# Optimization experiments

Hardware: AMD Instinct MI355X
Metric: run time of the kernel (lower is better)

The kernel has to match this reference:

```python
import jax, jax.numpy as jnp
import numpy as np

EMB = 256
N_NODES = 20000
N_EDGES = 200000


def _sage_layer(x, src, dst, edge_attr, W, b, n_nodes):
    # message = x[src] + edge_attr ; mean-aggregate into dst ; ReLU(Linear([x;agg]))
    msg = x[src] + edge_attr                                   # [2E, emb]
    s = jax.ops.segment_sum(msg, dst, num_segments=n_nodes)    # [N, emb]
    cnt = jax.ops.segment_sum(jnp.ones((dst.shape[0], 1), x.dtype), dst,
                              num_segments=n_nodes)            # [N, 1]
    agg = s / jnp.maximum(cnt, 1.0)
    return jax.nn.relu(jnp.concatenate([x, agg], axis=1) @ W + b)


def setup_inputs() -> dict:
    key = jax.random.key(0)
    ks = jax.random.split(key, 12)
    sc = 0.05
    inp = {
        "x": jax.random.normal(ks[0], (N_NODES, EMB), jnp.float32),
        "edge_attr": jax.random.normal(ks[1], (N_EDGES, EMB), jnp.float32),
        "batch_q_embds": jax.random.normal(ks[2], (N_EDGES, EMB), jnp.float32),
        "edge_index": jax.random.randint(ks[3], (2, N_EDGES), 0, N_NODES, jnp.int64
                                         if jax.config.jax_enable_x64 else jnp.int32),
        "W_rev1": jax.random.normal(ks[4], (EMB, EMB), jnp.float32) * sc,
        "b_rev1": jnp.zeros((EMB,), jnp.float32),
        "W_rev2": jax.random.normal(ks[5], (EMB, EMB), jnp.float32) * sc,
        "b_rev2": jnp.zeros((EMB,), jnp.float32),
        "W_sage1": jax.random.normal(ks[6], (2 * EMB, EMB), jnp.float32) * sc,
        "b_sage1": jnp.zeros((EMB,), jnp.float32),
        "W_sage2": jax.random.normal(ks[7], (2 * EMB, EMB), jnp.float32) * sc,
        "b_sage2": jnp.zeros((EMB,), jnp.float32),
        "W_pred1": jax.random.normal(ks[8], (6 * EMB, EMB), jnp.float32) * sc,
        "b_pred1": jnp.zeros((EMB,), jnp.float32),
        "W_pred2": jax.random.normal(ks[9], (EMB, 1), jnp.float32) * sc,
        "b_pred2": jnp.zeros((1,), jnp.float32),
    }
    return inp


def reference(x, edge_attr, batch_q_embds, edge_index,
              W_rev1, b_rev1, W_rev2, b_rev2,
              W_sage1, b_sage1, W_sage2, b_sage2,
              W_pred1, b_pred1, W_pred2, b_pred2):
    src, dst = edge_index[0], edge_index[1]
    # reverse-edge attributes via proj_reverse MLP
    edge_attr_rev = jax.nn.relu(edge_attr @ W_rev1 + b_rev1) @ W_rev2 + b_rev2
    src_f = jnp.concatenate([src, dst])          # [2E]
    dst_f = jnp.concatenate([dst, src])          # [2E]
    ea_f = jnp.concatenate([edge_attr, edge_attr_rev], axis=0)  # [2E, emb]
    # 2-layer GraphSAGE backbone over nodes, collect per-layer outputs
    h1 = _sage_layer(x, src_f, dst_f, ea_f, W_sage1, b_sage1, N_NODES)
    h2 = _sage_layer(h1, src_f, dst_f, ea_f, W_sage2, b_sage2, N_NODES)
    h_e = jnp.concatenate([h1, h2], axis=1)      # [N, 2*emb]
    # per-edge triple features: [q ; h_e[head] ; edge_attr ; h_e[tail]]
    h_triple = jnp.concatenate([batch_q_embds, h_e[src], edge_attr, h_e[dst]], axis=1)
    attn_logits = (jax.nn.relu(h_triple @ W_pred1 + b_pred1) @ W_pred2 + b_pred2)[:, 0]
    # idp-bern sampling (training=True): gumbel-like logistic noise, temp=1
    u = jax.random.uniform(jax.random.key(42), attn_logits.shape,
                           attn_logits.dtype, 1e-10, 1.0 - 1e-10)
    noise = jnp.log(u) - jnp.log(1.0 - u)
    sampled = jax.nn.sigmoid(attn_logits + noise)
    return attn_logits, sampled
```

## Files before the change

kernel.cpp:

```cpp
#include <hip/hip_runtime.h>
#include <cstdint>
#include <cstddef>

#define EMB 256
#define NN 20000
#define NE 200000
#define NE2 400000

typedef unsigned short ushort_t;
typedef __attribute__((ext_vector_type(8))) short bf16x8;
typedef __attribute__((ext_vector_type(4))) float f32x4;

__device__ __forceinline__ ushort_t f2bf(float f) {
    unsigned u = __float_as_uint(f);
    u += 0x7FFFu + ((u >> 16) & 1u);
    return (ushort_t)(u >> 16);
}
__device__ __forceinline__ float bf2f(ushort_t u) {
    return __uint_as_float(((unsigned)u) << 16);
}

__device__ __forceinline__ void async_cp16(const ushort_t* g, ushort_t* l) {
    __builtin_amdgcn_global_load_lds(
        (const __attribute__((address_space(1))) unsigned int*)g,
        (__attribute__((address_space(3))) unsigned int*)l,
        16, 0, 0);
}

__device__ __forceinline__ void pc_map(int bid, int T, int& p, int& colblk) {
    int Tf = T & ~15;
    if (bid < Tf) {
        p = (bid >> 4) * 8 + (bid & 7);
        colblk = (bid >> 3) & 1;
    } else {
        int rem = bid - Tf;
        int nr = (T - Tf) >> 1;
        p = (T >> 1) - nr + rem % nr;
        colblk = rem / nr;
    }
}

__device__ __forceinline__ unsigned rotl32(unsigned v, int d) {
    return (v << d) | (v >> (32 - d));
}
__device__ __forceinline__ void threefry2x32(unsigned k0, unsigned k1,
                                             unsigned x0, unsigned x1,
                                             unsigned& o0, unsigned& o1) {
    unsigned k2 = k0 ^ k1 ^ 0x1BD11BDAu;
    x0 += k0; x1 += k1;
#define TF_R(r) { x0 += x1; x1 = rotl32(x1, (r)); x1 ^= x0; }
    TF_R(13) TF_R(15) TF_R(26) TF_R(6)
    x0 += k1; x1 += k2 + 1u;
    TF_R(17) TF_R(29) TF_R(16) TF_R(24)
    x0 += k2; x1 += k0 + 2u;
    TF_R(13) TF_R(15) TF_R(26) TF_R(6)
    x0 += k0; x1 += k1 + 3u;
    TF_R(17) TF_R(29) TF_R(16) TF_R(24)
    x0 += k1; x1 += k2 + 4u;
    TF_R(13) TF_R(15) TF_R(26) TF_R(6)
    x0 += k2; x1 += k0 + 5u;
#undef TF_R
    o0 = x0; o1 = x1;
}

__global__ void deg_kernel(const int* __restrict__ src, const int* __restrict__ dst,
                           int* __restrict__ deg) {
    int i = blockIdx.x * blockDim.x + threadIdx.x;
    if (i < NE2) {
        int n = (i < NE) ? dst[i] : src[i - NE];
        atomicAdd(&deg[n], 1);
    }
}

__global__ void prefix_kernel(const int* __restrict__ deg, int* __restrict__ row_start,
                              int* __restrict__ cursor) {
    __shared__ int sums[1024];
    int t = threadIdx.x;
    const int CH = (NN + 1023) / 1024;
    int lo = t * CH, hi = lo + CH;
    if (hi > NN) hi = NN;
    if (lo > NN) lo = NN;
    int s = 0;
    for (int n = lo; n < hi; n++) s += deg[n];
    sums[t] = s;
    __syncthreads();
    for (int off = 1; off < 1024; off <<= 1) {
        int v = (t >= off) ? sums[t - off] : 0;
        __syncthreads();
        sums[t] += v;
        __syncthreads();
    }
    int run = (t == 0) ? 0 : sums[t - 1];
    for (int n = lo; n < hi; n++) {
        row_start[n] = run;
        cursor[n] = run;
        run += deg[n];
    }
    if (t == 1023) row_start[NN] = sums[1023];
}

__global__ void scatter_kernel(const int* __restrict__ src, const int* __restrict__ dst,
                               int* __restrict__ cursor, int* __restrict__ elist) {
    int i = blockIdx.x * blockDim.x + threadIdx.x;
    if (i < NE2) {
        int n = (i < NE) ? dst[i] : src[i - NE];
        int pos = atomicAdd(&cursor[n], 1);
        elist[pos] = i;
    }
}

__global__ void conv2_kernel(const float* __restrict__ a, ushort_t* __restrict__ oa, int na8,
                             const float* __restrict__ b, ushort_t* __restrict__ ob, int nb8) {
    int i = blockIdx.x * 256 + threadIdx.x;
    const float* p;
    ushort_t* o;
    if (i < na8) { p = a + (size_t)i * 8; o = oa + (size_t)i * 8; }
    else {
        int j = i - na8;
        if (j >= nb8) return;
        p = b + (size_t)j * 8; o = ob + (size_t)j * 8;
    }
    float4 u = *(const float4*)p;
    float4 v = *(const float4*)(p + 4);
    union { ushort_t s[8]; uint4 w; } r;
    r.s[0] = f2bf(u.x); r.s[1] = f2bf(u.y); r.s[2] = f2bf(u.z); r.s[3] = f2bf(u.w);
    r.s[4] = f2bf(v.x); r.s[5] = f2bf(v.y); r.s[6] = f2bf(v.z); r.s[7] = f2bf(v.w);
    *(uint4*)o = r.w;
}

struct TD { const float* src; ushort_t* dst; int stride, koff, kr; };
struct TA { TD d[8]; };

__global__ void transpose_all_kernel(TA ta) {
    TD t = ta.d[blockIdx.y];
    int k = blockIdx.x;
    if (k >= t.kr) return;
    int n = threadIdx.x;
    t.dst[(size_t)n * t.stride + t.koff + k] = f2bf(t.src[(size_t)k * 256 + n]);
}

template <int KTOT, int EPI, bool A0F32>
__global__ __launch_bounds__(256, 4) void mfma_gemm(
        const void* __restrict__ A0v, int rsA0,
        const ushort_t* __restrict__ A1, int rsA1,
        const ushort_t* __restrict__ Bt, const ushort_t* __restrict__ Bt2,
        const float* __restrict__ bias,
        void* __restrict__ out, void* __restrict__ out2, int rsOut, int M,
        const int* __restrict__ srcp, const int* __restrict__ dstp,
        const float* __restrict__ Hs, const float* __restrict__ Hd,
        const float* __restrict__ w2) {
    __shared__ ushort_t As[2][128 * 32];
    __shared__ ushort_t Bs[2][128 * 32];
    __shared__ float red[128];

    int tid = threadIdx.x;
    int lane = tid & 63;
    int wave = tid >> 6;
    int wr = wave >> 1;
    int wc = wave & 1;
    int quad = lane >> 4;
    int col_l = lane & 15;
    int p, colblk;
    pc_map(blockIdx.x, gridDim.x, p, colblk);

    const ushort_t* Bsel = blockIdx.y ? Bt2 : Bt;
    void* Osel = blockIdx.y ? out2 : out;

    f32x4 acc[4][4];
#pragma unroll
    for (int mt = 0; mt < 4; mt++)
#pragma unroll
        for (int nt = 0; nt < 4; nt++) acc[mt][nt] = (f32x4)0.f;

    for (int k0 = 0; k0 < KTOT; k0 += 64) {
        __syncthreads();
#pragma unroll
        for (int h = 0; h < 2; h++) {
            int kk = k0 + 32 * h;
#pragma unroll
            for (int j = 0; j < 2; j++) {
                int flat = tid + 256 * j;
                int n = flat >> 2, ch = flat & 3;
                const ushort_t* gp = Bsel + (size_t)(colblk * 128 + n) * KTOT + kk + ch * 8;
                async_cp16(gp, Bs[h] + ((wave * 64 + 256 * j) * 8));
            }
            bool seg1 = (KTOT == 512) && (kk >= 256);
            if (A0F32 && !seg1) {
#pragma unroll
                for (int j = 0; j < 2; j++) {
                    int flat = tid + 256 * j;
                    int row = flat >> 2, ch = flat & 3;
                    int grow = p * 128 + row;
                    if (grow >= M) grow = M - 1;
                    const float* gp = (const float*)A0v + (size_t)grow * rsA0 + kk + ch * 8;
                    float4 u = *(const float4*)gp;
                    float4 v = *(const float4*)(gp + 4);
                    union { ushort_t s[8]; uint4 w; } r;
                    r.s[0] = f2bf(u.x); r.s[1] = f2bf(u.y); r.s[2] = f2bf(u.z); r.s[3] = f2bf(u.w);
                    r.s[4] = f2bf(v.x); r.s[5] = f2bf(v.y); r.s[6] = f2bf(v.z); r.s[7] = f2bf(v.w);
                    *(uint4*)(As[h] + (size_t)flat * 8) = r.w;
                }
            } else {
                const ushort_t* abase;
                int rs, koffs;
                if (KTOT == 512 && kk >= 256) { abase = A1; rs = rsA1; koffs = kk - 256; }
                else { abase = (const ushort_t*)A0v; rs = rsA0; koffs = kk; }
#pragma unroll
                for (int j = 0; j < 2; j++) {
                    int flat = tid + 256 * j;
                    int row = flat >> 2, ch = flat & 3;
                    int grow = p * 128 + row;
                    if (grow >= M) grow = M - 1;
                    const ushort_t* gp = abase + (size_t)grow * rs + koffs + ch * 8;
                    async_cp16(gp, As[h] + ((wave * 64 + 256 * j) * 8));
                }
            }
        }
        __syncthreads();

#pragma unroll
        for (int h = 0; h < 2; h++) {
            bf16x8 a[4], b[4];
#pragma unroll
            for (int mt = 0; mt < 4; mt++)
                a[mt] = *(const bf16x8*)(As[h] + (wr * 64 + mt * 16 + col_l) * 32 + quad * 8);
#pragma unroll
            for (int nt = 0; nt < 4; nt++)
                b[nt] = *(const bf16x8*)(Bs[h] + (wc * 64 + nt * 16 + col_l) * 32 + quad * 8);
#pragma unroll
            for (int mt = 0; mt < 4; mt++)
#pragma unroll
                for (int nt = 0; nt < 4; nt++)
                    acc[mt][nt] = __builtin_amdgcn_mfma_f32_16x16x32_bf16(
                        a[mt], b[nt], acc[mt][nt], 0, 0, 0);
        }
    }

    if (EPI == 4) {
        __syncthreads();
        if (tid < 128) red[tid] = 0.f;
        __syncthreads();
        float b1c[4], w2c[4];
#pragma unroll
        for (int nt = 0; nt < 4; nt++) {
            int col = colblk * 128 + wc * 64 + nt * 16 + col_l;
            b1c[nt] = bias[col];
            w2c[nt] = w2[col];
        }
#pragma unroll
        for (int mt = 0; mt < 4; mt++) {
#pragma unroll
            for (int r = 0; r < 4; r++) {
                int lrow = wr * 64 + mt * 16 + quad * 4 + r;
                int e = p * 128 + lrow;
                int ec = e < M ? e : M - 1;
                int s = srcp[ec], d = dstp[ec];
                const float* hsr = Hs + (size_t)s * 256;
                const float* hdr = Hd + (size_t)d * 256;
                float part = 0.f;
#pragma unroll
                for (int nt = 0; nt < 4; nt++) {
                    int col = colblk * 128 + wc * 64 + nt * 16 + col_l;
                    part += fmaxf(acc[mt][nt][r] + hsr[col] + hdr[col] + b1c[nt], 0.f)
                            * w2c[nt];
                }
#pragma unroll
                for (int m = 8; m > 0; m >>= 1) part += __shfl_xor(part, m, 64);
                if (col_l == 0) atomicAdd(&red[lrow], part);
            }
        }
        __syncthreads();
        if (tid < 128) {
            int e = p * 128 + tid;
            if (e < M) {
                float* tgt = colblk ? (float*)out2 : (float*)out;
                tgt[e] = red[tid];
            }
        }
        return;
    }

    float bs[4];
    if (EPI >= 2) {
#pragma unroll
        for (int nt = 0; nt < 4; nt++)
            bs[nt] = bias[colblk * 128 + wc * 64 + nt * 16 + col_l];
    }
#pragma unroll
    for (int mt = 0; mt < 4; mt++) {
#pragma unroll
        for (int nt = 0; nt < 4; nt++) {
            int colg = colblk * 128 + wc * 64 + nt * 16 + col_l;
#pragma unroll
            for (int r = 0; r < 4; r++) {
                int rg = p * 128 + wr * 64 + mt * 16 + quad * 4 + r;
                if (rg < M) {
                    float v = acc[mt][nt][r];
                    if (EPI >= 2) v += bs[nt];
                    if (EPI == 3) v = fmaxf(v, 0.f);
                    if (EPI == 0)
                        ((float*)Osel)[(size_t)rg * rsOut + colg] = v;
                    else
                        ((ushort_t*)Osel)[(size_t)rg * rsOut + colg] = f2bf(v);
                }
            }
        }
    }
}

__global__ void finalize_kernel(float* __restrict__ out, const float* __restrict__ part1,
                                const float* __restrict__ b2v, float* __restrict__ out_s) {
    int e = blockIdx.x * blockDim.x + threadIdx.x;
    if (e >= NE) return;
    float logit = out[e] + part1[e] + b2v[0];
    out[e] = logit;
    unsigned y0, y1;
    threefry2x32(0u, 42u, 0u, (unsigned)e, y0, y1);
    unsigned bits = y0 ^ y1;
    float f = __uint_as_float((bits >> 9) | 0x3F800000u) - 1.0f;
    float u = fmaxf(1e-10f, f + 1e-10f);
    float noise = logf(u) - logf(1.0f - u);
    out_s[e] = 1.0f / (1.0f + expf(-(logit + noise)));
}

__global__ __launch_bounds__(64) void agg_ea_kernel(
        const ushort_t* __restrict__ eaf, const ushort_t* __restrict__ ear,
        const int* __restrict__ row_start, const int* __restrict__ elist,
        float* __restrict__ agg_ea) {
    int n = blockIdx.x;
    int c = threadIdx.x * 4;
    float ax = 0.f, ay = 0.f, az = 0.f, aw = 0.f;
    int beg = row_start[n], end = row_start[n + 1];
    for (int p = beg; p < end; p++) {
        int i = elist[p];
        const ushort_t* er = (i < NE) ? eaf + (size_t)i * 256
                                      : ear + (size_t)(i - NE) * 256;
        ushort4 ev = *(const ushort4*)(er + c);
        ax += bf2f(ev.x); ay += bf2f(ev.y); az += bf2f(ev.z); aw += bf2f(ev.w);
    }
    float4 o; o.x = ax; o.y = ay; o.z = az; o.w = aw;
    *(float4*)(agg_ea + (size_t)n * 256 + c) = o;
}

__global__ __launch_bounds__(64) void agg_x_kernel(
        const ushort_t* __restrict__ xin, int rsx,
        const int* __restrict__ src, const int* __restrict__ dst,
        const int* __restrict__ row_start, const int* __restrict__ elist,
        const int* __restrict__ deg, const float* __restrict__ agg_ea,
        ushort_t* __restrict__ agg) {
    int n = blockIdx.x;
    int c = threadIdx.x * 4;
    float ax = 0.f, ay = 0.f, az = 0.f, aw = 0.f;
    int beg = row_start[n], end = row_start[n + 1];
    for (int p = beg; p < end; p++) {
        int i = elist[p];
        int node = (i < NE) ? src[i] : dst[i - NE];
        ushort4 xv = *(const ushort4*)(xin + (size_t)node * rsx + c);
        ax += bf2f(xv.x); ay += bf2f(xv.y); az += bf2f(xv.z); aw += bf2f(xv.w);
    }
    float4 e = *(const float4*)(agg_ea + (size_t)n * 256 + c);
    float d = fmaxf((float)deg[n], 1.0f);
    ushort4 o;
    o.x = f2bf((ax + e.x) / d); o.y = f2bf((ay + e.y) / d);
    o.z = f2bf((az + e.z) / d); o.w = f2bf((aw + e.w) / d);
    *(ushort4*)(agg + (size_t)n * 256 + c) = o;
}

extern "C" void kernel_launch(void* const* d_in, const int* in_sizes, int n_in,
                              void* d_out, int out_size, void* d_ws, size_t ws_size,
                              hipStream_t stream) {
    const float* x        = (const float*)d_in[0];
    const float* ea       = (const float*)d_in[1];
    const float* qemb     = (const float*)d_in[2];
    const int*   eidx     = (const int*)d_in[3];
    const float* W_rev1   = (const float*)d_in[4];
    const float* b_rev1   = (const float*)d_in[5];
    const float* W_rev2   = (const float*)d_in[6];
    const float* b_rev2   = (const float*)d_in[7];
    const float* W_sage1  = (const float*)d_in[8];
    const float* b_sage1  = (const float*)d_in[9];
    const float* W_sage2  = (const float*)d_in[10];
    const float* b_sage2  = (const float*)d_in[11];
    const float* W_pred1  = (const float*)d_in[12];
    const float* b_pred1  = (const float*)d_in[13];
    const float* W_pred2  = (const float*)d_in[14];
    const float* b_pred2  = (const float*)d_in[15];
    float* out = (float*)d_out;

    const int* src = eidx;
    const int* dst = eidx + NE;

    char* w = (char*)d_ws;
    ushort_t* ea_bf  = (ushort_t*)w; w += (size_t)NE * 256 * 2;
    ushort_t* hid_bf = (ushort_t*)w; w += (size_t)NE * 256 * 2;
    ushort_t* ea_rev_bf = (ushort_t*)w; w += (size_t)NE * 256 * 2;
    ushort_t* x_bf   = (ushort_t*)w; w += (size_t)NN * 256 * 2;
    ushort_t* H      = (ushort_t*)w; w += (size_t)NN * 512 * 2;
    ushort_t* agg_bf = (ushort_t*)w; w += (size_t)NN * 256 * 2;
    float*    Hsrc   = (float*)w;    w += (size_t)NN * 256 * 4;
    float*    Hdst   = (float*)w;    w += (size_t)NN * 256 * 4;
    float*    part1  = (float*)w;    w += (size_t)NE * 4;
    ushort_t* Wt_rev1  = (ushort_t*)w; w += 256 * 256 * 2;
    ushort_t* Wt_rev2  = (ushort_t*)w; w += 256 * 256 * 2;
    ushort_t* Wt_sage1 = (ushort_t*)w; w += 256 * 512 * 2;
    ushort_t* Wt_sage2 = (ushort_t*)w; w += 256 * 512 * 2;
    ushort_t* Wt_src   = (ushort_t*)w; w += 256 * 512 * 2;
    ushort_t* Wt_dst   = (ushort_t*)w; w += 256 * 512 * 2;
    ushort_t* Wt_edge  = (ushort_t*)w; w += 256 * 512 * 2;
    int* deg       = (int*)w; w += (size_t)NN * 4;
    int* row_start = (int*)w; w += (size_t)(NN + 1) * 4;
    int* cursor    = (int*)w; w += (size_t)NN * 4;
    int* elist     = (int*)w; w += (size_t)NE2 * 4;

    float* agg_ea = Hsrc;

    const int EB = (NE + 127) / 128;
    const int NB = (NN + 127) / 128;

    hipMemsetAsync(deg, 0, (size_t)NN * 4, stream);
    deg_kernel<<<(NE2 + 255) / 256, 256, 0, stream>>>(src, dst, deg);
    prefix_kernel<<<1, 1024, 0, stream>>>(deg, row_start, cursor);
    scatter_kernel<<<(NE2 + 255) / 256, 256, 0, stream>>>(src, dst, cursor, elist);

    TA ta;
    ta.d[0] = { W_rev1,  Wt_rev1,  256, 0,   256 };
    ta.d[1] = { W_rev2,  Wt_rev2,  256, 0,   256 };
    ta.d[2] = { W_sage1, Wt_sage1, 512, 0,   512 };
    ta.d[3] = { W_sage2, Wt_sage2, 512, 0,   512 };
    ta.d[4] = { W_pred1 + (size_t)256 * 256,  Wt_src,  512, 0,   512 };
    ta.d[5] = { W_pred1 + (size_t)1024 * 256, Wt_dst,  512, 0,   512 };
    ta.d[6] = { W_pred1,                      Wt_edge, 512, 0,   256 };
    ta.d[7] = { W_pred1 + (size_t)768 * 256,  Wt_edge, 512, 256, 256 };
    transpose_all_kernel<<<dim3(512, 8), 256, 0, stream>>>(ta);

    conv2_kernel<<<((NE + NN) * 32 + 255) / 256, 256, 0, stream>>>(
        ea, ea_bf, NE * 32, x, x_bf, NN * 32);

    mfma_gemm<256, 3, false><<<EB * 2, 256, 0, stream>>>(
        ea_bf, 256, nullptr, 0, Wt_rev1, nullptr, b_rev1,
        hid_bf, nullptr, 256, NE, nullptr, nullptr, nullptr, nullptr, nullptr);
    mfma_gemm<256, 2, false><<<EB * 2, 256, 0, stream>>>(
        hid_bf, 256, nullptr, 0, Wt_rev2, nullptr, b_rev2,
        ea_rev_bf, nullptr, 256, NE, nullptr, nullptr, nullptr, nullptr, nullptr);

    agg_ea_kernel<<<NN, 64, 0, stream>>>(ea_bf, ea_rev_bf, row_start, elist, agg_ea);

    agg_x_kernel<<<NN, 64, 0, stream>>>(x_bf, 256, src, dst, row_start, elist,
                                        deg, agg_ea, agg_bf);
    mfma_gemm<512, 3, false><<<NB * 2, 256, 0, stream>>>(
        x_bf, 256, agg_bf, 256, Wt_sage1, nullptr, b_sage1,
        H, nullptr, 512, NN, nullptr, nullptr, nullptr, nullptr, nullptr);

    agg_x_kernel<<<NN, 64, 0, stream>>>(H, 512, src, dst, row_start, elist,
                                        deg, agg_ea, agg_bf);
    mfma_gemm<512, 3, false><<<NB * 2, 256, 0, stream>>>(
        H, 512, agg_bf, 256, Wt_sage2, nullptr, b_sage2,
        H + 256, nullptr, 512, NN, nullptr, nullptr, nullptr, nullptr, nullptr);

    mfma_gemm<512, 0, false><<<dim3(NB * 2, 2), 256, 0, stream>>>(
        H, 512, H + 256, 512, Wt_src, Wt_dst, nullptr,
        Hsrc, Hdst, 256, NN, nullptr, nullptr, nullptr, nullptr, nullptr);

    mfma_gemm<512, 4, true><<<EB * 2, 256, 0, stream>>>(
        qemb, 256, ea_bf, 256, Wt_edge, nullptr, b_pred1,
        out, part1, 0, NE, src, dst, Hsrc, Hdst, W_pred2);

    finalize_kernel<<<(NE + 255) / 256, 256, 0, stream>>>(out, part1, b_pred2, out + NE);
}
```

Baseline: 978.5 us.

## Fuse reverse-edge two-layer MLP into one kernel keeping hidden tile in LDS

Replaces the two back-to-back GEMM launches for the proj_reverse MLP with a single kernel. Each block handles 64 edge rows, computes the first layer plus ReLU into an LDS-resident bf16 hidden tile, then runs the second GEMM from LDS. This removes the global write and read of the 200000x256 hidden intermediate and one launch. In exchange it uses a smaller M tile with no double buffering, and the full weight matrix is reloaded per block, which may reduce MFMA efficiency.

```diff
diff --git a/kernel.cpp b/kernel.cpp
--- a/kernel.cpp
+++ b/kernel.cpp
@@ -137,6 +137,115 @@
     if (k >= t.kr) return;
     int n = threadIdx.x;
     t.dst[(size_t)n * t.stride + t.koff + k] = f2bf(t.src[(size_t)k * 256 + n]);
+}
+
+__global__ __launch_bounds__(256, 3) void rev_fused_kernel(
+        const ushort_t* __restrict__ ea_bf,
+        const ushort_t* __restrict__ Wt1, const float* __restrict__ b1,
+        const ushort_t* __restrict__ Wt2, const float* __restrict__ b2,
+        ushort_t* __restrict__ ea_rev) {
+    __shared__ ushort_t As[64 * 32];
+    __shared__ ushort_t Bs[256 * 32];
+    __shared__ ushort_t Hl[64 * 264];
+
+    int tid = threadIdx.x;
+    int lane = tid & 63, wave = tid >> 6;
+    int wr = wave >> 1, wc = wave & 1;
+    int quad = lane >> 4, col_l = lane & 15;
+    int p = blockIdx.x;
+
+    f32x4 acc[2][8];
+#pragma unroll
+    for (int mt = 0; mt < 2; mt++)
+#pragma unroll
+        for (int nt = 0; nt < 8; nt++) acc[mt][nt] = (f32x4)0.f;
+
+    for (int k0 = 0; k0 < 256; k0 += 32) {
+        __syncthreads();
+        {
+            int row = tid >> 2, ch = tid & 3;
+            async_cp16(ea_bf + (size_t)(p * 64 + row) * 256 + k0 + ch * 8,
+                       As + (wave * 64) * 8);
+        }
+#pragma unroll
+        for (int j = 0; j < 4; j++) {
+            int flat = tid + 256 * j;
+            int n = flat >> 2, ch = flat & 3;
+            async_cp16(Wt1 + (size_t)n * 256 + k0 + ch * 8,
+                       Bs + (wave * 64 + 256 * j) * 8);
+        }
+        __syncthreads();
+        bf16x8 a[2], b[8];
+#pragma unroll
+        for (int mt = 0; mt < 2; mt++)
+            a[mt] = *(const bf16x8*)(As + (wr * 32 + mt * 16 + col_l) * 32 + quad * 8);
+#pragma unroll
+        for (int nt = 0; nt < 8; nt++)
+            b[nt] = *(const bf16x8*)(Bs + (wc * 128 + nt * 16 + col_l) * 32 + quad * 8);
+#pragma unroll
+        for (int mt = 0; mt < 2; mt++)
+#pragma unroll
+            for (int nt = 0; nt < 8; nt++)
+                acc[mt][nt] = __builtin_amdgcn_mfma_f32_16x16x32_bf16(
+                    a[mt], b[nt], acc[mt][nt], 0, 0, 0);
+    }
+
+    __syncthreads();
+#pragma unroll
+    for (int nt = 0; nt < 8; nt++) {
+        int lcol = wc * 128 + nt * 16 + col_l;
+        float bb = b1[lcol];
+#pragma unroll
+        for (int mt = 0; mt < 2; mt++)
+#pragma unroll
+            for (int r = 0; r < 4; r++) {
+                int lrow = wr * 32 + mt * 16 + quad * 4 + r;
+                Hl[lrow * 264 + lcol] = f2bf(fmaxf(acc[mt][nt][r] + bb, 0.f));
+            }
+    }
+#pragma unroll
+    for (int mt = 0; mt < 2; mt++)
+#pragma unroll
+        for (int nt = 0; nt < 8; nt++) acc[mt][nt] = (f32x4)0.f;
+
+    for (int k0 = 0; k0 < 256; k0 += 32) {
+        __syncthreads();
+#pragma unroll
+        for (int j = 0; j < 4; j++) {
+            int flat = tid + 256 * j;
+            int n = flat >> 2, ch = flat & 3;
+            async_cp16(Wt2 + (size_t)n * 256 + k0 + ch * 8,
+                       Bs + (wave * 64 + 256 * j) * 8);
+        }
+        __syncthreads();
+        bf16x8 a[2], b[8];
+#pragma unroll
+        for (int mt = 0; mt < 2; mt++)
+            a[mt] = *(const bf16x8*)(Hl + (wr * 32 + mt * 16 + col_l) * 264
+                                     + k0 + quad * 8);
+#pragma unroll
+        for (int nt = 0; nt < 8; nt++)
+            b[nt] = *(const bf16x8*)(Bs + (wc * 128 + nt * 16 + col_l) * 32 + quad * 8);
+#pragma unroll
+        for (int mt = 0; mt < 2; mt++)
+#pragma unroll
+            for (int nt = 0; nt < 8; nt++)
+                acc[mt][nt] = __builtin_amdgcn_mfma_f32_16x16x32_bf16(
+                    a[mt], b[nt], acc[mt][nt], 0, 0, 0);
+    }
+
+#pragma unroll
+    for (int nt = 0; nt < 8; nt++) {
+        int colg = wc * 128 + nt * 16 + col_l;
+        float bb = b2[colg];
+#pragma unroll
+        for (int mt = 0; mt < 2; mt++)
+#pragma unroll
+            for (int r = 0; r < 4; r++) {
+                int rg = p * 64 + wr * 32 + mt * 16 + quad * 4 + r;
+                ea_rev[(size_t)rg * 256 + colg] = f2bf(acc[mt][nt][r] + bb);
+            }
+    }
 }
 
 template <int KTOT, int EPI, bool A0F32>
@@ -392,7 +501,6 @@
 
     char* w = (char*)d_ws;
     ushort_t* ea_bf  = (ushort_t*)w; w += (size_t)NE * 256 * 2;
-    ushort_t* hid_bf = (ushort_t*)w; w += (size_t)NE * 256 * 2;
     ushort_t* ea_rev_bf = (ushort_t*)w; w += (size_t)NE * 256 * 2;
     ushort_t* x_bf   = (ushort_t*)w; w += (size_t)NN * 256 * 2;
     ushort_t* H      = (ushort_t*)w; w += (size_t)NN * 512 * 2;
@@ -436,12 +544,8 @@
     conv2_kernel<<<((NE + NN) * 32 + 255) / 256, 256, 0, stream>>>(
         ea, ea_bf, NE * 32, x, x_bf, NN * 32);
 
-    mfma_gemm<256, 3, false><<<EB * 2, 256, 0, stream>>>(
-        ea_bf, 256, nullptr, 0, Wt_rev1, nullptr, b_rev1,
-        hid_bf, nullptr, 256, NE, nullptr, nullptr, nullptr, nullptr, nullptr);
-    mfma_gemm<256, 2, false><<<EB * 2, 256, 0, stream>>>(
-        hid_bf, 256, nullptr, 0, Wt_rev2, nullptr, b_rev2,
-        ea_rev_bf, nullptr, 256, NE, nullptr, nullptr, nullptr, nullptr, nullptr);
+    rev_fused_kernel<<<NE / 64, 256, 0, stream>>>(
+        ea_bf, Wt_rev1, b_rev1, Wt_rev2, b_rev2, ea_rev_bf);
 
     agg_ea_kernel<<<NN, 64, 0, stream>>>(ea_bf, ea_rev_bf, row_start, elist, agg_ea);
 
```

Result: faster. 951.9 us (-2.7%).
